# Performance work log

Hardware: AMD Instinct MI355X
Metric: run time of the kernel (lower is better)

Reference implementation:

```python
import jax, jax.numpy as jnp
import numpy as np

N_EMBD = 2048
N_HEAD = 16
D_HEAD = N_EMBD // N_HEAD


def setup_inputs() -> dict:
    key = jax.random.key(0)
    k1, k2, k3 = jax.random.split(key, 3)
    x = jax.random.normal(k1, (2, 2048, N_EMBD), dtype=jnp.float32)
    # torch Linear stores weight as [out, in]; kept in that layout
    w_qkv = jax.random.normal(k2, (3 * N_EMBD, N_EMBD), dtype=jnp.float32) * (1.0 / np.sqrt(N_EMBD))
    w_out = jax.random.normal(k3, (N_EMBD, N_EMBD), dtype=jnp.float32) * (1.0 / np.sqrt(N_EMBD))
    return {"x": x, "w_qkv": w_qkv, "w_out": w_out}


def reference(x, w_qkv, w_out):
    B, T, C = x.shape
    H, D = N_HEAD, D_HEAD
    qkv = jnp.einsum('btc,oc->bto', x, w_qkv)            # [B,T,3C]
    qkv = qkv.reshape(B, T, 3, H, D)
    q = jnp.transpose(qkv[:, :, 0], (0, 2, 1, 3))        # [B,H,T,D]
    k = jnp.transpose(qkv[:, :, 1], (0, 2, 1, 3))
    v = jnp.transpose(qkv[:, :, 2], (0, 2, 1, 3))
    scale = 1.0 / np.sqrt(D).astype(np.float32)
    att = jnp.einsum('bhqd,bhkd->bhqk', q, k) * scale    # [B,H,T,T]
    causal = jnp.tril(jnp.ones((T, T), dtype=bool))
    att = jnp.where(causal[None, None], att, jnp.finfo(att.dtype).min)
    att = jax.nn.softmax(att, axis=-1)
    y = jnp.einsum('bhqk,bhkd->bhqd', att, v)            # [B,H,T,D]
    y = jnp.transpose(y, (0, 2, 1, 3)).reshape(B, T, C)
    return jnp.einsum('btc,oc->bto', y, w_out)
```

## Files before the change

kernel.cpp:

```cpp
#include <hip/hip_runtime.h>
#include <stdint.h>


typedef __attribute__((ext_vector_type(8))) short bf16x8;
typedef __attribute__((ext_vector_type(8))) unsigned short u16x8;
typedef __attribute__((ext_vector_type(4))) unsigned short u16x4;
typedef __attribute__((ext_vector_type(4))) float f32x4;

#define MFMA16(a, b, c) __builtin_amdgcn_mfma_f32_16x16x32_bf16((a), (b), (c), 0, 0, 0)

__device__ __forceinline__ unsigned short f2bf(float f) {
  union { float f; uint32_t u; } v; v.f = f;
  uint32_t r = v.u + 0x7FFFu + ((v.u >> 16) & 1u);
  return (unsigned short)(r >> 16);
}

__device__ __forceinline__ void gld_lds16(const unsigned short* g, unsigned short* lds) {
  __builtin_amdgcn_global_load_lds(
      (const __attribute__((address_space(1))) void*)g,
      (__attribute__((address_space(3))) void*)lds, 16, 0, 0);
}

__global__ __launch_bounds__(256) void cvt_bf16(const float* __restrict__ in,
                                                unsigned short* __restrict__ out, int n8) {
  int stride = gridDim.x * blockDim.x;
  for (int i = blockIdx.x * blockDim.x + threadIdx.x; i < n8; i += stride) {
    float4 a = reinterpret_cast<const float4*>(in)[i * 2];
    float4 b = reinterpret_cast<const float4*>(in)[i * 2 + 1];
    u16x8 o;
    o[0] = f2bf(a.x); o[1] = f2bf(a.y); o[2] = f2bf(a.z); o[3] = f2bf(a.w);
    o[4] = f2bf(b.x); o[5] = f2bf(b.y); o[6] = f2bf(b.z); o[7] = f2bf(b.w);
    reinterpret_cast<u16x8*>(out)[i] = o;
  }
}

__device__ __forceinline__ void gemm128_core(const unsigned short* __restrict__ A,
                                             const unsigned short* __restrict__ Bt,
                                             int K, int brow, int bcol,
                                             unsigned short* lds_a, unsigned short* lds_b,
                                             f32x4 acc[4][4]) {
  const int tid = threadIdx.x;
  const int l   = tid & 63;
  const int w   = tid >> 6;
  const int wr  = (w >> 1) << 6;
  const int wc  = (w & 1) << 6;

  const int srow = tid >> 2;
  const int sswz = (tid & 3) ^ ((srow >> 1) & 3);
  const unsigned short* gA0 = A  + (size_t)(brow + srow) * K + 8 * sswz;
  const unsigned short* gA1 = gA0 + (size_t)64 * K;
  const unsigned short* gB0 = Bt + (size_t)(bcol + srow) * K + 8 * sswz;
  const unsigned short* gB1 = gB0 + (size_t)64 * K;

  unsigned short* la0 = lds_a + tid * 8;
  unsigned short* la1 = lds_a + (256 + tid) * 8;
  unsigned short* lb0 = lds_b + tid * 8;
  unsigned short* lb1 = lds_b + (256 + tid) * 8;

  const int fm    = l & 15;
  const int fswz8 = 8 * ((l >> 4) ^ ((fm >> 1) & 3));

  for (int k0 = 0; k0 < K; k0 += 32) {
    gld_lds16(gA0, la0);
    gld_lds16(gA1, la1);
    gld_lds16(gB0, lb0);
    gld_lds16(gB1, lb1);
    gA0 += 32; gA1 += 32; gB0 += 32; gB1 += 32;
    __syncthreads();
    bf16x8 af[4], bfv[4];
#pragma unroll
    for (int i = 0; i < 4; i++)
      af[i] = *(const bf16x8*)&lds_a[(wr + i * 16 + fm) * 32 + fswz8];
#pragma unroll
    for (int j = 0; j < 4; j++)
      bfv[j] = *(const bf16x8*)&lds_b[(wc + j * 16 + fm) * 32 + fswz8];
#pragma unroll
    for (int i = 0; i < 4; i++)
#pragma unroll
      for (int j = 0; j < 4; j++)
        acc[i][j] = MFMA16(af[i], bfv[j], acc[i][j]);
    __syncthreads();
  }
}

__global__ __launch_bounds__(256) void gemm_qkv(const unsigned short* __restrict__ xb,
                                                const unsigned short* __restrict__ wqb,
                                                unsigned short* __restrict__ Qb,
                                                unsigned short* __restrict__ Kb,
                                                unsigned short* __restrict__ Vtb) {
  __shared__ alignas(16) unsigned short lds_a[128 * 32];
  __shared__ alignas(16) unsigned short lds_b[128 * 32];
  f32x4 acc[4][4];
#pragma unroll
  for (int i = 0; i < 4; i++)
#pragma unroll
    for (int j = 0; j < 4; j++) acc[i][j] = (f32x4){0.f, 0.f, 0.f, 0.f};

  const int brow = blockIdx.y << 7;
  const int bcol = blockIdx.x << 7;
  gemm128_core(xb, wqb, 2048, brow, bcol, lds_a, lds_b, acc);

  const int l = threadIdx.x & 63;
  const int w = threadIdx.x >> 6;
  const int wr = (w >> 1) << 6, wc = (w & 1) << 6;
  const int which = bcol >> 11;
  const int bh = ((brow >> 11) << 4) | ((bcol >> 7) & 15);
  const int tbase = (brow & 2047) + wr + ((l >> 4) << 2);

#pragma unroll
  for (int i = 0; i < 4; i++) {
    const int t0 = tbase + i * 16;
#pragma unroll
    for (int j = 0; j < 4; j++) {
      const int d = wc + j * 16 + (l & 15);
      if (which == 2) {
        u16x4 pk;
#pragma unroll
        for (int r = 0; r < 4; r++) pk[r] = f2bf(acc[i][j][r]);
        *reinterpret_cast<u16x4*>(&Vtb[((size_t)bh * 128 + d) * 2048 + t0]) = pk;
      } else {
        unsigned short* dst = (which == 0 ? Qb : Kb) + ((size_t)bh * 2048 + t0) * 128 + d;
#pragma unroll
        for (int r = 0; r < 4; r++) dst[(size_t)r * 128] = f2bf(acc[i][j][r]);
      }
    }
  }
}

__global__ __launch_bounds__(256) void gemm_out(const unsigned short* __restrict__ yb,
                                                const unsigned short* __restrict__ wob,
                                                float* __restrict__ out) {
  __shared__ alignas(16) unsigned short lds_a[128 * 32];
  __shared__ alignas(16) unsigned short lds_b[128 * 32];
  f32x4 acc[4][4];
#pragma unroll
  for (int i = 0; i < 4; i++)
#pragma unroll
    for (int j = 0; j < 4; j++) acc[i][j] = (f32x4){0.f, 0.f, 0.f, 0.f};

  const int brow = blockIdx.y << 7;
  const int bcol = blockIdx.x << 7;
  gemm128_core(yb, wob, 2048, brow, bcol, lds_a, lds_b, acc);

  const int l = threadIdx.x & 63;
  const int w = threadIdx.x >> 6;
  const int wr = (w >> 1) << 6, wc = (w & 1) << 6;
#pragma unroll
  for (int i = 0; i < 4; i++) {
    const int m0 = brow + wr + i * 16 + ((l >> 4) << 2);
#pragma unroll
    for (int j = 0; j < 4; j++) {
      const int n = bcol + wc + j * 16 + (l & 15);
#pragma unroll
      for (int r = 0; r < 4; r++) out[(size_t)(m0 + r) * 2048 + n] = acc[i][j][r];
    }
  }
}

__global__ __launch_bounds__(256) void attn_kernel(const unsigned short* __restrict__ Qb,
                                                   const unsigned short* __restrict__ Kb,
                                                   const unsigned short* __restrict__ Vtb,
                                                   unsigned short* __restrict__ Yb) {
  __shared__ alignas(16) unsigned short lds_k[64 * 128];
  __shared__ alignas(16) unsigned short lds_v[128 * 64];
  __shared__ alignas(16) unsigned short p_lds[4][16 * 64];

  const int tid = threadIdx.x;
  const int l = tid & 63;
  const int w = tid >> 6;
  const int bh = blockIdx.y;
  const int b = bh >> 4, h = bh & 15;
  const float SC = 0.12752585f;

  const unsigned short* Qg = Qb + (size_t)bh * 2048 * 128;
  const unsigned short* Kg = Kb + (size_t)bh * 2048 * 128;
  const unsigned short* Vg = Vtb + (size_t)bh * 128 * 2048;

  for (int ph = 0; ph < 2; ph++) {
    const int h64 = (ph == 0) ? (int)blockIdx.x : (31 - (int)blockIdx.x);
    const int q0 = h64 << 6;
    const int qw0 = q0 + (w << 4);

    bf16x8 qf[4];
#pragma unroll
    for (int ds = 0; ds < 4; ds++)
      qf[ds] = *(const bf16x8*)&Qg[(size_t)(qw0 + (l & 15)) * 128 + ds * 32 + 8 * (l >> 4)];

    f32x4 yacc[8];
#pragma unroll
    for (int dt = 0; dt < 8; dt++) yacc[dt] = (f32x4){0.f, 0.f, 0.f, 0.f};
    float mrow[4], lrow[4];
#pragma unroll
    for (int r = 0; r < 4; r++) { mrow[r] = -1e30f; lrow[r] = 0.f; }

    const int nkv = h64 + 1;
    for (int t = 0; t < nkv; t++) {
      const int kv0 = t << 6;
#pragma unroll
      for (int c = 0; c < 4; c++) {
        int s = c * 256 + tid;
        int row = s >> 4, g = s & 15;
        gld_lds16(&Kg[(size_t)(kv0 + row) * 128 + 8 * (g ^ (row & 7))], &lds_k[s * 8]);
      }
#pragma unroll
      for (int c = 0; c < 4; c++) {
        int s = c * 256 + tid;
        int row = s >> 3, g = s & 7;
        gld_lds16(&Vg[(size_t)row * 2048 + kv0 + 8 * (g ^ (row & 7))], &lds_v[s * 8]);
      }
      __syncthreads();

      if (kv0 <= qw0 + 15) {
        f32x4 sfr[4];
#pragma unroll
        for (int kt = 0; kt < 4; kt++) {
          const int kr = kt * 16 + (l & 15);
          f32x4 s4 = (f32x4){0.f, 0.f, 0.f, 0.f};
#pragma unroll
          for (int ds = 0; ds < 4; ds++) {
            bf16x8 kfr = *(const bf16x8*)&lds_k[kr * 128 + 8 * (((ds << 2) + (l >> 4)) ^ (kr & 7))];
            s4 = MFMA16(qf[ds], kfr, s4);
          }
          sfr[kt] = s4;
        }
        const bool need_mask = (kv0 + 63 > qw0);
#pragma unroll
        for (int kt = 0; kt < 4; kt++)
#pragma unroll
          for (int r = 0; r < 4; r++) {
            float sv = sfr[kt][r] * SC;
            if (need_mask) {
              int qa = qw0 + ((l >> 4) << 2) + r;
              int ka = kv0 + kt * 16 + (l & 15);
              sv = (ka > qa) ? -1e30f : sv;
            }
            sfr[kt][r] = sv;
          }
        float rmax, f[4], rsum[4];
#pragma unroll
        for (int r = 0; r < 4; r++) {
          rmax = fmaxf(fmaxf(sfr[0][r], sfr[1][r]), fmaxf(sfr[2][r], sfr[3][r]));
          rmax = fmaxf(rmax, __shfl_xor(rmax, 1));
          rmax = fmaxf(rmax, __shfl_xor(rmax, 2));
          rmax = fmaxf(rmax, __shfl_xor(rmax, 4));
          rmax = fmaxf(rmax, __shfl_xor(rmax, 8));
          float mn = fmaxf(mrow[r], rmax);
          f[r] = exp2f(mrow[r] - mn);
          mrow[r] = mn;
          rsum[r] = 0.f;
        }
#pragma unroll
        for (int kt = 0; kt < 4; kt++)
#pragma unroll
          for (int r = 0; r < 4; r++) {
            float p = exp2f(sfr[kt][r] - mrow[r]);
            rsum[r] += p;
            int row = ((l >> 4) << 2) + r;
            int k = kt * 16 + (l & 15);
            p_lds[w][row * 64 + (((k >> 3) ^ (row & 7)) << 3) + (k & 7)] = f2bf(p);
          }
#pragma unroll
        for (int r = 0; r < 4; r++) {
          float s = rsum[r];
          s += __shfl_xor(s, 1);
          s += __shfl_xor(s, 2);
          s += __shfl_xor(s, 4);
          s += __shfl_xor(s, 8);
          lrow[r] = lrow[r] * f[r] + s;
        }
#pragma unroll
        for (int dt = 0; dt < 8; dt++)
#pragma unroll
          for (int r = 0; r < 4; r++) yacc[dt][r] *= f[r];

        asm volatile("s_waitcnt lgkmcnt(0)" ::: "memory");
        __builtin_amdgcn_sched_barrier(0);

#pragma unroll
        for (int ks = 0; ks < 2; ks++) {
          const int prow = l & 15;
          bf16x8 pa = *(const bf16x8*)&p_lds[w][prow * 64 + ((((ks << 2) + (l >> 4)) ^ (prow & 7)) << 3)];
#pragma unroll
          for (int dt = 0; dt < 8; dt++) {
            const int d = dt * 16 + (l & 15);
            bf16x8 vb = *(const bf16x8*)&lds_v[d * 64 + ((((ks << 2) + (l >> 4)) ^ (d & 7)) << 3)];
            yacc[dt] = MFMA16(pa, vb, yacc[dt]);
          }
        }
      }
      __syncthreads();
    }
#pragma unroll
    for (int dt = 0; dt < 8; dt++)
#pragma unroll
      for (int r = 0; r < 4; r++) {
        int qa = qw0 + ((l >> 4) << 2) + r;
        Yb[((size_t)(b * 2048 + qa)) * 2048 + h * 128 + dt * 16 + (l & 15)] =
            f2bf(yacc[dt][r] / lrow[r]);
      }
  }
}

extern "C" void kernel_launch(void* const* d_in, const int* in_sizes, int n_in,
                              void* d_out, int out_size, void* d_ws, size_t ws_size,
                              hipStream_t stream) {
  const float* x    = (const float*)d_in[0];
  const float* wqkv = (const float*)d_in[1];
  const float* wout = (const float*)d_in[2];
  float* out = (float*)d_out;

  unsigned short* ws  = (unsigned short*)d_ws;
  unsigned short* xb  = ws;
  unsigned short* wqb = xb + (size_t)8388608;
  unsigned short* wob = wqb + (size_t)12582912;
  unsigned short* Qb  = wob + (size_t)4194304;
  unsigned short* Kb  = Qb + (size_t)8388608;
  unsigned short* Vtb = Kb + (size_t)8388608;
  unsigned short* Yb  = Vtb + (size_t)8388608;

  cvt_bf16<<<1024, 256, 0, stream>>>(x, xb, 8388608 / 8);
  cvt_bf16<<<1024, 256, 0, stream>>>(wqkv, wqb, 12582912 / 8);
  cvt_bf16<<<512, 256, 0, stream>>>(wout, wob, 4194304 / 8);
  gemm_qkv<<<dim3(48, 32), 256, 0, stream>>>(xb, wqb, Qb, Kb, Vtb);
  attn_kernel<<<dim3(16, 32), 256, 0, stream>>>(Qb, Kb, Vtb, Yb);
  gemm_out<<<dim3(16, 32), 256, 0, stream>>>(Yb, wob, out);
}
```

Before: 291.4 us.

## Replace QKV GEMM with 256x256-tile, 8-wave, multi-stage pipelined kernel

The QKV projection GEMM now uses 256x256 output tiles computed by 512 threads (8 waves). It replaces the single-buffered 128x128 kernel with a double-buffered, K-split LDS pipeline that issues global-to-LDS loads ahead of the MFMA phases, using explicit vmcnt waits, sched barriers and s_setprio. A block-index swizzle groups tiles for L2 reuse. The aim is to hide load latency and raise arithmetic intensity per LDS byte, at the cost of more LDS (128 KB per block), more accumulator registers, fewer blocks (384), and a fragile hand-written wait schedule; the LDS layout drops the bank-conflict swizzle of the old kernel.

```diff
diff --git a/kernel.cpp b/kernel.cpp
--- a/kernel.cpp
+++ b/kernel.cpp
@@ -6,6 +6,7 @@
 typedef __attribute__((ext_vector_type(8))) unsigned short u16x8;
 typedef __attribute__((ext_vector_type(4))) unsigned short u16x4;
 typedef __attribute__((ext_vector_type(4))) float f32x4;
+typedef unsigned short ushort_t;
 
 #define MFMA16(a, b, c) __builtin_amdgcn_mfma_f32_16x16x32_bf16((a), (b), (c), 0, 0, 0)
 
@@ -19,6 +20,12 @@
   __builtin_amdgcn_global_load_lds(
       (const __attribute__((address_space(1))) void*)g,
       (__attribute__((address_space(3))) void*)lds, 16, 0, 0);
+}
+
+__device__ __forceinline__ void sbar() {
+  __builtin_amdgcn_sched_barrier(0);
+  __builtin_amdgcn_s_barrier();
+  __builtin_amdgcn_sched_barrier(0);
 }
 
 __global__ __launch_bounds__(256) void cvt_bf16(const float* __restrict__ in,
@@ -34,6 +41,131 @@
   }
 }
 
+#define QNT 32
+
+#define STG_A(DBUF, KSS, KOFF)                                                  \
+  do { gld_lds16(gA0 + (KOFF), lA + ((DBUF)*2 + (KSS)) * 8192 + tid * 8);       \
+       gld_lds16(gA1 + (KOFF), lA + ((DBUF)*2 + (KSS)) * 8192 + 4096 + tid * 8); } while (0)
+#define STG_B(DBUF, KSS, KOFF)                                                  \
+  do { gld_lds16(gB0 + (KOFF), lB + ((DBUF)*2 + (KSS)) * 8192 + tid * 8);       \
+       gld_lds16(gB1 + (KOFF), lB + ((DBUF)*2 + (KSS)) * 8192 + 4096 + tid * 8); } while (0)
+
+#define PH(BUF, KS, MG, STAGE_STMT, WAIT_STMT)                                  \
+  {                                                                             \
+    const unsigned short* lab = lA + ((BUF) * 2 + (KS)) * 8192;                 \
+    const unsigned short* lbb = lB + ((BUF) * 2 + (KS)) * 8192;                 \
+    bf16x8 af_[4];                                                              \
+    _Pragma("unroll") for (int mf = 0; mf < 4; ++mf)                            \
+      af_[mf] = *(const bf16x8*)&lab[(wm * 128 + (MG) * 64 + mf * 16 + lm) * 32 + k8]; \
+    if ((MG) == 0) {                                                            \
+      _Pragma("unroll") for (int nf = 0; nf < 4; ++nf)                          \
+        bfr[nf] = *(const bf16x8*)&lbb[(wn * 64 + nf * 16 + lm) * 32 + k8];     \
+    }                                                                           \
+    STAGE_STMT;                                                                 \
+    sbar();                                                                     \
+    asm volatile("s_waitcnt lgkmcnt(0)" ::: "memory");                          \
+    __builtin_amdgcn_sched_barrier(0);                                          \
+    __builtin_amdgcn_s_setprio(1);                                              \
+    _Pragma("unroll") for (int mf = 0; mf < 4; ++mf)                            \
+      _Pragma("unroll") for (int nf = 0; nf < 4; ++nf)                          \
+        acc[(MG) * 4 + mf][nf] = MFMA16(af_[mf], bfr[nf], acc[(MG) * 4 + mf][nf]); \
+    __builtin_amdgcn_s_setprio(0);                                              \
+    WAIT_STMT;                                                                  \
+    sbar();                                                                     \
+  }
+
+#define WV8 asm volatile("s_waitcnt vmcnt(8)" ::: "memory")
+#define WV4 asm volatile("s_waitcnt vmcnt(4)" ::: "memory")
+#define WV0 asm volatile("s_waitcnt vmcnt(0)" ::: "memory")
+#define NOPST ((void)0)
+
+__global__ __launch_bounds__(512, 2) void gemm_qkv8(const unsigned short* __restrict__ xb,
+                                                    const unsigned short* __restrict__ wqb,
+                                                    unsigned short* __restrict__ Qb,
+                                                    unsigned short* __restrict__ Kb,
+                                                    unsigned short* __restrict__ Vtb) {
+  __shared__ alignas(16) unsigned short lA[2 * 2 * 8192];
+  __shared__ alignas(16) unsigned short lB[2 * 2 * 8192];
+
+  const int bid = blockIdx.x;
+  const int swz = (bid & 7) * 48 + (bid >> 3);
+  const int bx = swz % 24, by = swz / 24;
+  const int brow = by << 8, bcol = bx << 8;
+
+  const int tid = threadIdx.x;
+  const int l = tid & 63, w = tid >> 6;
+  const int wm = w >> 2, wn = w & 3;
+  const int lm = l & 15, k8 = 8 * (l >> 4);
+
+  const int srow = tid >> 2;
+  const int sk8 = (tid & 3) * 8;
+  const unsigned short* gA0 = xb + (size_t)(brow + srow) * 2048 + sk8;
+  const unsigned short* gA1 = xb + (size_t)(brow + 128 + srow) * 2048 + sk8;
+  const unsigned short* gB0 = wqb + (size_t)(bcol + srow) * 2048 + sk8;
+  const unsigned short* gB1 = wqb + (size_t)(bcol + 128 + srow) * 2048 + sk8;
+
+  f32x4 acc[8][4];
+#pragma unroll
+  for (int i = 0; i < 8; ++i)
+#pragma unroll
+    for (int j = 0; j < 4; ++j) acc[i][j] = (f32x4){0.f, 0.f, 0.f, 0.f};
+  bf16x8 bfr[4];
+
+  STG_A(0, 0, 0);  STG_B(0, 0, 0);
+  STG_A(0, 1, 32); STG_B(0, 1, 32);
+  STG_A(1, 0, 64); STG_B(1, 0, 64);
+  WV8;
+  sbar();
+
+  for (int t = 0; t < QNT - 2; ++t) {
+    const int buf = t & 1;
+    PH(buf, 0, 0, STG_A(buf ^ 1, 1, (t + 1) * 64 + 32), NOPST);
+    PH(buf, 0, 1, STG_B(buf ^ 1, 1, (t + 1) * 64 + 32), WV8);
+    PH(buf, 1, 0, STG_A(buf, 0, (t + 2) * 64), NOPST);
+    PH(buf, 1, 1, STG_B(buf, 0, (t + 2) * 64), WV8);
+  }
+  {
+    const int buf = (QNT - 2) & 1;
+    PH(buf, 0, 0, STG_A(buf ^ 1, 1, (QNT - 1) * 64 + 32), NOPST);
+    PH(buf, 0, 1, STG_B(buf ^ 1, 1, (QNT - 1) * 64 + 32), WV8);
+    PH(buf, 1, 0, NOPST, NOPST);
+    PH(buf, 1, 1, NOPST, WV4);
+  }
+  {
+    const int buf = (QNT - 1) & 1;
+    PH(buf, 0, 0, NOPST, NOPST);
+    PH(buf, 0, 1, NOPST, WV0);
+    PH(buf, 1, 0, NOPST, NOPST);
+    PH(buf, 1, 1, NOPST, NOPST);
+  }
+
+  const int lr4 = (l >> 4) << 2;
+#pragma unroll
+  for (int mf = 0; mf < 8; ++mf) {
+    const int trow = brow + wm * 128 + mf * 16 + lr4;
+    const int b_ = trow >> 11;
+    const int t0 = trow & 2047;
+#pragma unroll
+    for (int nf = 0; nf < 4; ++nf) {
+      const int c = bcol + wn * 64 + nf * 16 + lm;
+      const int which = c >> 11;
+      const int cc = c & 2047;
+      const int h = cc >> 7, d = cc & 127;
+      const int bh = (b_ << 4) | h;
+      if (which == 2) {
+        u16x4 pk;
+#pragma unroll
+        for (int r = 0; r < 4; ++r) pk[r] = f2bf(acc[mf][nf][r]);
+        *reinterpret_cast<u16x4*>(&Vtb[((size_t)bh * 128 + d) * 2048 + t0]) = pk;
+      } else {
+        unsigned short* dst = (which == 0 ? Qb : Kb) + ((size_t)bh * 2048 + t0) * 128 + d;
+#pragma unroll
+        for (int r = 0; r < 4; ++r) dst[(size_t)r * 128] = f2bf(acc[mf][nf][r]);
+      }
+    }
+  }
+}
+
 __device__ __forceinline__ void gemm128_core(const unsigned short* __restrict__ A,
                                              const unsigned short* __restrict__ Bt,
                                              int K, int brow, int bcol,
@@ -80,50 +212,6 @@
       for (int j = 0; j < 4; j++)
         acc[i][j] = MFMA16(af[i], bfv[j], acc[i][j]);
     __syncthreads();
-  }
-}
-
-__global__ __launch_bounds__(256) void gemm_qkv(const unsigned short* __restrict__ xb,
-                                                const unsigned short* __restrict__ wqb,
-                                                unsigned short* __restrict__ Qb,
-                                                unsigned short* __restrict__ Kb,
-                                                unsigned short* __restrict__ Vtb) {
-  __shared__ alignas(16) unsigned short lds_a[128 * 32];
-  __shared__ alignas(16) unsigned short lds_b[128 * 32];
-  f32x4 acc[4][4];
-#pragma unroll
-  for (int i = 0; i < 4; i++)
-#pragma unroll
-    for (int j = 0; j < 4; j++) acc[i][j] = (f32x4){0.f, 0.f, 0.f, 0.f};
-
-  const int brow = blockIdx.y << 7;
-  const int bcol = blockIdx.x << 7;
-  gemm128_core(xb, wqb, 2048, brow, bcol, lds_a, lds_b, acc);
-
-  const int l = threadIdx.x & 63;
-  const int w = threadIdx.x >> 6;
-  const int wr = (w >> 1) << 6, wc = (w & 1) << 6;
-  const int which = bcol >> 11;
-  const int bh = ((brow >> 11) << 4) | ((bcol >> 7) & 15);
-  const int tbase = (brow & 2047) + wr + ((l >> 4) << 2);
-
-#pragma unroll
-  for (int i = 0; i < 4; i++) {
-    const int t0 = tbase + i * 16;
-#pragma unroll
-    for (int j = 0; j < 4; j++) {
-      const int d = wc + j * 16 + (l & 15);
-      if (which == 2) {
-        u16x4 pk;
-#pragma unroll
-        for (int r = 0; r < 4; r++) pk[r] = f2bf(acc[i][j][r]);
-        *reinterpret_cast<u16x4*>(&Vtb[((size_t)bh * 128 + d) * 2048 + t0]) = pk;
-      } else {
-        unsigned short* dst = (which == 0 ? Qb : Kb) + ((size_t)bh * 2048 + t0) * 128 + d;
-#pragma unroll
-        for (int r = 0; r < 4; r++) dst[(size_t)r * 128] = f2bf(acc[i][j][r]);
-      }
-    }
   }
 }
 
@@ -321,7 +409,7 @@
   cvt_bf16<<<1024, 256, 0, stream>>>(x, xb, 8388608 / 8);
   cvt_bf16<<<1024, 256, 0, stream>>>(wqkv, wqb, 12582912 / 8);
   cvt_bf16<<<512, 256, 0, stream>>>(wout, wob, 4194304 / 8);
-  gemm_qkv<<<dim3(48, 32), 256, 0, stream>>>(xb, wqb, Qb, Kb, Vtb);
+  gemm_qkv8<<<384, 512, 0, stream>>>(xb, wqb, Qb, Kb, Vtb);
   attn_kernel<<<dim3(16, 32), 256, 0, stream>>>(Qb, Kb, Vtb, Yb);
   gemm_out<<<dim3(16, 32), 256, 0, stream>>>(Yb, wob, out);
 }
```

Result: slower. 333.7 us (+14.5%).

## Double-buffer GEMM LDS loads, remap blocks per XCD, and split attention query tiles

Applied to the files above, without the earlier changes.

Both GEMMs now use double-buffered LDS, so the global-to-LDS copy of the next K slice runs while MFMAs work on the current one. All three kernels switch to a flat 1D grid with an XCD-aware block-to-tile mapping, so tiles sharing operands (or the same head) land on the same XCD and reuse its L2. The attention kernel drops the per-block pairing of two query tiles (one short, one long) and launches one block per query tile, staggering tile order by head. This adds parallelism and cache locality but gives up the built-in causal load balancing, and doubles GEMM LDS use, which may lower occupancy.

```diff
diff --git a/kernel.cpp b/kernel.cpp
--- a/kernel.cpp
+++ b/kernel.cpp
@@ -34,51 +34,62 @@
   }
 }
 
-__device__ __forceinline__ void gemm128_core(const unsigned short* __restrict__ A,
+#define STG128(BUFOFF, KOFF)                                                    \
+  do {                                                                          \
+    gld_lds16(gA0 + (KOFF), ldsA + (BUFOFF) + tid * 8);                         \
+    gld_lds16(gA1 + (KOFF), ldsA + (BUFOFF) + 2048 + tid * 8);                  \
+    gld_lds16(gB0 + (KOFF), ldsB + (BUFOFF) + tid * 8);                         \
+    gld_lds16(gB1 + (KOFF), ldsB + (BUFOFF) + 2048 + tid * 8);                  \
+  } while (0)
+
+__device__ __forceinline__ void gemm128_step(const unsigned short* la,
+                                             const unsigned short* lb,
+                                             int wr, int wc, int fm, int fswz8,
+                                             f32x4 acc[4][4]) {
+  bf16x8 af[4], bfv[4];
+#pragma unroll
+  for (int i = 0; i < 4; i++)
+    af[i] = *(const bf16x8*)&la[(wr + i * 16 + fm) * 32 + fswz8];
+#pragma unroll
+  for (int j = 0; j < 4; j++)
+    bfv[j] = *(const bf16x8*)&lb[(wc + j * 16 + fm) * 32 + fswz8];
+#pragma unroll
+  for (int i = 0; i < 4; i++)
+#pragma unroll
+    for (int j = 0; j < 4; j++)
+      acc[i][j] = MFMA16(af[i], bfv[j], acc[i][j]);
+}
+
+__device__ __forceinline__ void gemm128_dbuf(const unsigned short* __restrict__ A,
                                              const unsigned short* __restrict__ Bt,
                                              int K, int brow, int bcol,
-                                             unsigned short* lds_a, unsigned short* lds_b,
+                                             unsigned short* ldsA, unsigned short* ldsB,
                                              f32x4 acc[4][4]) {
   const int tid = threadIdx.x;
-  const int l   = tid & 63;
-  const int w   = tid >> 6;
-  const int wr  = (w >> 1) << 6;
-  const int wc  = (w & 1) << 6;
+  const int l = tid & 63;
+  const int w = tid >> 6;
+  const int wr = (w >> 1) << 6;
+  const int wc = (w & 1) << 6;
 
   const int srow = tid >> 2;
   const int sswz = (tid & 3) ^ ((srow >> 1) & 3);
-  const unsigned short* gA0 = A  + (size_t)(brow + srow) * K + 8 * sswz;
+  const unsigned short* gA0 = A + (size_t)(brow + srow) * K + 8 * sswz;
   const unsigned short* gA1 = gA0 + (size_t)64 * K;
   const unsigned short* gB0 = Bt + (size_t)(bcol + srow) * K + 8 * sswz;
   const unsigned short* gB1 = gB0 + (size_t)64 * K;
 
-  unsigned short* la0 = lds_a + tid * 8;
-  unsigned short* la1 = lds_a + (256 + tid) * 8;
-  unsigned short* lb0 = lds_b + tid * 8;
-  unsigned short* lb1 = lds_b + (256 + tid) * 8;
-
-  const int fm    = l & 15;
+  const int fm = l & 15;
   const int fswz8 = 8 * ((l >> 4) ^ ((fm >> 1) & 3));
 
-  for (int k0 = 0; k0 < K; k0 += 32) {
-    gld_lds16(gA0, la0);
-    gld_lds16(gA1, la1);
-    gld_lds16(gB0, lb0);
-    gld_lds16(gB1, lb1);
-    gA0 += 32; gA1 += 32; gB0 += 32; gB1 += 32;
+  STG128(0, 0);
+  __syncthreads();
+
+  for (int k0 = 0; k0 < K; k0 += 64) {
+    STG128(4096, k0 + 32);
+    gemm128_step(ldsA, ldsB, wr, wc, fm, fswz8, acc);
     __syncthreads();
-    bf16x8 af[4], bfv[4];
-#pragma unroll
-    for (int i = 0; i < 4; i++)
-      af[i] = *(const bf16x8*)&lds_a[(wr + i * 16 + fm) * 32 + fswz8];
-#pragma unroll
-    for (int j = 0; j < 4; j++)
-      bfv[j] = *(const bf16x8*)&lds_b[(wc + j * 16 + fm) * 32 + fswz8];
-#pragma unroll
-    for (int i = 0; i < 4; i++)
-#pragma unroll
-      for (int j = 0; j < 4; j++)
-        acc[i][j] = MFMA16(af[i], bfv[j], acc[i][j]);
+    if (k0 + 64 < K) STG128(0, k0 + 64);
+    gemm128_step(ldsA + 4096, ldsB + 4096, wr, wc, fm, fswz8, acc);
     __syncthreads();
   }
 }
@@ -88,17 +99,23 @@
                                                 unsigned short* __restrict__ Qb,
                                                 unsigned short* __restrict__ Kb,
                                                 unsigned short* __restrict__ Vtb) {
-  __shared__ alignas(16) unsigned short lds_a[128 * 32];
-  __shared__ alignas(16) unsigned short lds_b[128 * 32];
+  __shared__ alignas(16) unsigned short ldsA[2 * 128 * 32];
+  __shared__ alignas(16) unsigned short ldsB[2 * 128 * 32];
   f32x4 acc[4][4];
 #pragma unroll
   for (int i = 0; i < 4; i++)
 #pragma unroll
     for (int j = 0; j < 4; j++) acc[i][j] = (f32x4){0.f, 0.f, 0.f, 0.f};
 
-  const int brow = blockIdx.y << 7;
-  const int bcol = blockIdx.x << 7;
-  gemm128_core(xb, wqb, 2048, brow, bcol, lds_a, lds_b, acc);
+  const int bid = blockIdx.x;
+  const int xcd = bid & 7;
+  const int loc = bid >> 3;
+  const int bx = xcd * 6 + loc % 6;
+  const int by = loc / 6;
+  const int brow = by << 7;
+  const int bcol = bx << 7;
+
+  gemm128_dbuf(xb, wqb, 2048, brow, bcol, ldsA, ldsB, acc);
 
   const int l = threadIdx.x & 63;
   const int w = threadIdx.x >> 6;
@@ -130,17 +147,23 @@
 __global__ __launch_bounds__(256) void gemm_out(const unsigned short* __restrict__ yb,
                                                 const unsigned short* __restrict__ wob,
                                                 float* __restrict__ out) {
-  __shared__ alignas(16) unsigned short lds_a[128 * 32];
-  __shared__ alignas(16) unsigned short lds_b[128 * 32];
+  __shared__ alignas(16) unsigned short ldsA[2 * 128 * 32];
+  __shared__ alignas(16) unsigned short ldsB[2 * 128 * 32];
   f32x4 acc[4][4];
 #pragma unroll
   for (int i = 0; i < 4; i++)
 #pragma unroll
     for (int j = 0; j < 4; j++) acc[i][j] = (f32x4){0.f, 0.f, 0.f, 0.f};
 
-  const int brow = blockIdx.y << 7;
-  const int bcol = blockIdx.x << 7;
-  gemm128_core(yb, wob, 2048, brow, bcol, lds_a, lds_b, acc);
+  const int bid = blockIdx.x;
+  const int xcd = bid & 7;
+  const int loc = bid >> 3;
+  const int bx = (xcd & 3) * 4 + (loc & 3);
+  const int by = (xcd >> 2) * 16 + (loc >> 2);
+  const int brow = by << 7;
+  const int bcol = bx << 7;
+
+  gemm128_dbuf(yb, wob, 2048, brow, bcol, ldsA, ldsB, acc);
 
   const int l = threadIdx.x & 63;
   const int w = threadIdx.x >> 6;
@@ -168,7 +191,14 @@
   const int tid = threadIdx.x;
   const int l = tid & 63;
   const int w = tid >> 6;
-  const int bh = blockIdx.y;
+
+  const int flat = blockIdx.x;
+  const int xcd = flat & 7;
+  const int loc = flat >> 3;
+  const int bh = xcd * 4 + (loc >> 5);
+  const int jidx = loc & 31;
+  const int h64 = (jidx + bh) & 31;
+
   const int b = bh >> 4, h = bh & 15;
   const float SC = 0.12752585f;
 
@@ -176,129 +206,126 @@
   const unsigned short* Kg = Kb + (size_t)bh * 2048 * 128;
   const unsigned short* Vg = Vtb + (size_t)bh * 128 * 2048;
 
-  for (int ph = 0; ph < 2; ph++) {
-    const int h64 = (ph == 0) ? (int)blockIdx.x : (31 - (int)blockIdx.x);
-    const int q0 = h64 << 6;
-    const int qw0 = q0 + (w << 4);
-
-    bf16x8 qf[4];
-#pragma unroll
-    for (int ds = 0; ds < 4; ds++)
-      qf[ds] = *(const bf16x8*)&Qg[(size_t)(qw0 + (l & 15)) * 128 + ds * 32 + 8 * (l >> 4)];
-
-    f32x4 yacc[8];
-#pragma unroll
-    for (int dt = 0; dt < 8; dt++) yacc[dt] = (f32x4){0.f, 0.f, 0.f, 0.f};
-    float mrow[4], lrow[4];
-#pragma unroll
-    for (int r = 0; r < 4; r++) { mrow[r] = -1e30f; lrow[r] = 0.f; }
-
-    const int nkv = h64 + 1;
-    for (int t = 0; t < nkv; t++) {
-      const int kv0 = t << 6;
-#pragma unroll
-      for (int c = 0; c < 4; c++) {
-        int s = c * 256 + tid;
-        int row = s >> 4, g = s & 15;
-        gld_lds16(&Kg[(size_t)(kv0 + row) * 128 + 8 * (g ^ (row & 7))], &lds_k[s * 8]);
-      }
-#pragma unroll
-      for (int c = 0; c < 4; c++) {
-        int s = c * 256 + tid;
-        int row = s >> 3, g = s & 7;
-        gld_lds16(&Vg[(size_t)row * 2048 + kv0 + 8 * (g ^ (row & 7))], &lds_v[s * 8]);
-      }
-      __syncthreads();
-
-      if (kv0 <= qw0 + 15) {
-        f32x4 sfr[4];
-#pragma unroll
-        for (int kt = 0; kt < 4; kt++) {
-          const int kr = kt * 16 + (l & 15);
-          f32x4 s4 = (f32x4){0.f, 0.f, 0.f, 0.f};
-#pragma unroll
-          for (int ds = 0; ds < 4; ds++) {
-            bf16x8 kfr = *(const bf16x8*)&lds_k[kr * 128 + 8 * (((ds << 2) + (l >> 4)) ^ (kr & 7))];
-            s4 = MFMA16(qf[ds], kfr, s4);
+  const int q0 = h64 << 6;
+  const int qw0 = q0 + (w << 4);
+
+  bf16x8 qf[4];
+#pragma unroll
+  for (int ds = 0; ds < 4; ds++)
+    qf[ds] = *(const bf16x8*)&Qg[(size_t)(qw0 + (l & 15)) * 128 + ds * 32 + 8 * (l >> 4)];
+
+  f32x4 yacc[8];
+#pragma unroll
+  for (int dt = 0; dt < 8; dt++) yacc[dt] = (f32x4){0.f, 0.f, 0.f, 0.f};
+  float mrow[4], lrow[4];
+#pragma unroll
+  for (int r = 0; r < 4; r++) { mrow[r] = -1e30f; lrow[r] = 0.f; }
+
+  const int nkv = h64 + 1;
+  for (int t = 0; t < nkv; t++) {
+    const int kv0 = t << 6;
+#pragma unroll
+    for (int c = 0; c < 4; c++) {
+      int s = c * 256 + tid;
+      int row = s >> 4, g = s & 15;
+      gld_lds16(&Kg[(size_t)(kv0 + row) * 128 + 8 * (g ^ (row & 7))], &lds_k[s * 8]);
+    }
+#pragma unroll
+    for (int c = 0; c < 4; c++) {
+      int s = c * 256 + tid;
+      int row = s >> 3, g = s & 7;
+      gld_lds16(&Vg[(size_t)row * 2048 + kv0 + 8 * (g ^ (row & 7))], &lds_v[s * 8]);
+    }
+    __syncthreads();
+
+    if (kv0 <= qw0 + 15) {
+      f32x4 sfr[4];
+#pragma unroll
+      for (int kt = 0; kt < 4; kt++) {
+        const int kr = kt * 16 + (l & 15);
+        f32x4 s4 = (f32x4){0.f, 0.f, 0.f, 0.f};
+#pragma unroll
+        for (int ds = 0; ds < 4; ds++) {
+          bf16x8 kfr = *(const bf16x8*)&lds_k[kr * 128 + 8 * (((ds << 2) + (l >> 4)) ^ (kr & 7))];
+          s4 = MFMA16(qf[ds], kfr, s4);
+        }
+        sfr[kt] = s4;
+      }
+      const bool need_mask = (kv0 + 63 > qw0);
+#pragma unroll
+      for (int kt = 0; kt < 4; kt++)
+#pragma unroll
+        for (int r = 0; r < 4; r++) {
+          float sv = sfr[kt][r] * SC;
+          if (need_mask) {
+            int qa = qw0 + ((l >> 4) << 2) + r;
+            int ka = kv0 + kt * 16 + (l & 15);
+            sv = (ka > qa) ? -1e30f : sv;
           }
-          sfr[kt] = s4;
+          sfr[kt][r] = sv;
         }
-        const bool need_mask = (kv0 + 63 > qw0);
-#pragma unroll
-        for (int kt = 0; kt < 4; kt++)
-#pragma unroll
-          for (int r = 0; r < 4; r++) {
-            float sv = sfr[kt][r] * SC;
-            if (need_mask) {
-              int qa = qw0 + ((l >> 4) << 2) + r;
-              int ka = kv0 + kt * 16 + (l & 15);
-              sv = (ka > qa) ? -1e30f : sv;
-            }
-            sfr[kt][r] = sv;
-          }
-        float rmax, f[4], rsum[4];
+      float rmax, f[4], rsum[4];
+#pragma unroll
+      for (int r = 0; r < 4; r++) {
+        rmax = fmaxf(fmaxf(sfr[0][r], sfr[1][r]), fmaxf(sfr[2][r], sfr[3][r]));
+        rmax = fmaxf(rmax, __shfl_xor(rmax, 1));
+        rmax = fmaxf(rmax, __shfl_xor(rmax, 2));
+        rmax = fmaxf(rmax, __shfl_xor(rmax, 4));
+        rmax = fmaxf(rmax, __shfl_xor(rmax, 8));
+        float mn = fmaxf(mrow[r], rmax);
+        f[r] = exp2f(mrow[r] - mn);
+        mrow[r] = mn;
+        rsum[r] = 0.f;
+      }
+#pragma unroll
+      for (int kt = 0; kt < 4; kt++)
 #pragma unroll
         for (int r = 0; r < 4; r++) {
-          rmax = fmaxf(fmaxf(sfr[0][r], sfr[1][r]), fmaxf(sfr[2][r], sfr[3][r]));
-          rmax = fmaxf(rmax, __shfl_xor(rmax, 1));
-          rmax = fmaxf(rmax, __shfl_xor(rmax, 2));
-          rmax = fmaxf(rmax, __shfl_xor(rmax, 4));
-          rmax = fmaxf(rmax, __shfl_xor(rmax, 8));
-          float mn = fmaxf(mrow[r], rmax);
-          f[r] = exp2f(mrow[r] - mn);
-          mrow[r] = mn;
-          rsum[r] = 0.f;
+          float p = exp2f(sfr[kt][r] - mrow[r]);
+          rsum[r] += p;
+          int row = ((l >> 4) << 2) + r;
+          int k = kt * 16 + (l & 15);
+          p_lds[w][row * 64 + (((k >> 3) ^ (row & 7)) << 3) + (k & 7)] = f2bf(p);
         }
 #pragma unroll
-        for (int kt = 0; kt < 4; kt++)
-#pragma unroll
-          for (int r = 0; r < 4; r++) {
-            float p = exp2f(sfr[kt][r] - mrow[r]);
-            rsum[r] += p;
-            int row = ((l >> 4) << 2) + r;
-            int k = kt * 16 + (l & 15);
-            p_lds[w][row * 64 + (((k >> 3) ^ (row & 7)) << 3) + (k & 7)] = f2bf(p);
-          }
-#pragma unroll
-        for (int r = 0; r < 4; r++) {
-          float s = rsum[r];
-          s += __shfl_xor(s, 1);
-          s += __shfl_xor(s, 2);
-          s += __shfl_xor(s, 4);
-          s += __shfl_xor(s, 8);
-          lrow[r] = lrow[r] * f[r] + s;
+      for (int r = 0; r < 4; r++) {
+        float s = rsum[r];
+        s += __shfl_xor(s, 1);
+        s += __shfl_xor(s, 2);
+        s += __shfl_xor(s, 4);
+        s += __shfl_xor(s, 8);
+        lrow[r] = lrow[r] * f[r] + s;
+      }
+#pragma unroll
+      for (int dt = 0; dt < 8; dt++)
+#pragma unroll
+        for (int r = 0; r < 4; r++) yacc[dt][r] *= f[r];
+
+      asm volatile("s_waitcnt lgkmcnt(0)" ::: "memory");
+      __builtin_amdgcn_sched_barrier(0);
+
+#pragma unroll
+      for (int ks = 0; ks < 2; ks++) {
+        const int prow = l & 15;
+        bf16x8 pa = *(const bf16x8*)&p_lds[w][prow * 64 + ((((ks << 2) + (l >> 4)) ^ (prow & 7)) << 3)];
+#pragma unroll
+        for (int dt = 0; dt < 8; dt++) {
+          const int d = dt * 16 + (l & 15);
+          bf16x8 vb = *(const bf16x8*)&lds_v[d * 64 + ((((ks << 2) + (l >> 4)) ^ (d & 7)) << 3)];
+          yacc[dt] = MFMA16(pa, vb, yacc[dt]);
         }
-#pragma unroll
-        for (int dt = 0; dt < 8; dt++)
-#pragma unroll
-          for (int r = 0; r < 4; r++) yacc[dt][r] *= f[r];
-
-        asm volatile("s_waitcnt lgkmcnt(0)" ::: "memory");
-        __builtin_amdgcn_sched_barrier(0);
-
-#pragma unroll
-        for (int ks = 0; ks < 2; ks++) {
-          const int prow = l & 15;
-          bf16x8 pa = *(const bf16x8*)&p_lds[w][prow * 64 + ((((ks << 2) + (l >> 4)) ^ (prow & 7)) << 3)];
-#pragma unroll
-          for (int dt = 0; dt < 8; dt++) {
-            const int d = dt * 16 + (l & 15);
-            bf16x8 vb = *(const bf16x8*)&lds_v[d * 64 + ((((ks << 2) + (l >> 4)) ^ (d & 7)) << 3)];
-            yacc[dt] = MFMA16(pa, vb, yacc[dt]);
-          }
-        }
-      }
-      __syncthreads();
-    }
-#pragma unroll
-    for (int dt = 0; dt < 8; dt++)
-#pragma unroll
-      for (int r = 0; r < 4; r++) {
-        int qa = qw0 + ((l >> 4) << 2) + r;
-        Yb[((size_t)(b * 2048 + qa)) * 2048 + h * 128 + dt * 16 + (l & 15)] =
-            f2bf(yacc[dt][r] / lrow[r]);
-      }
-  }
+      }
+    }
+    __syncthreads();
+  }
+#pragma unroll
+  for (int dt = 0; dt < 8; dt++)
+#pragma unroll
+    for (int r = 0; r < 4; r++) {
+      int qa = qw0 + ((l >> 4) << 2) + r;
+      Yb[((size_t)(b * 2048 + qa)) * 2048 + h * 128 + dt * 16 + (l & 15)] =
+          f2bf(yacc[dt][r] / lrow[r]);
+    }
 }
 
 extern "C" void kernel_launch(void* const* d_in, const int* in_sizes, int n_in,
@@ -321,7 +348,7 @@
   cvt_bf16<<<1024, 256, 0, stream>>>(x, xb, 8388608 / 8);
   cvt_bf16<<<1024, 256, 0, stream>>>(wqkv, wqb, 12582912 / 8);
   cvt_bf16<<<512, 256, 0, stream>>>(wout, wob, 4194304 / 8);
-  gemm_qkv<<<dim3(48, 32), 256, 0, stream>>>(xb, wqb, Qb, Kb, Vtb);
-  attn_kernel<<<dim3(16, 32), 256, 0, stream>>>(Qb, Kb, Vtb, Yb);
-  gemm_out<<<dim3(16, 32), 256, 0, stream>>>(Yb, wob, out);
-}
+  gemm_qkv<<<1536, 256, 0, stream>>>(xb, wqb, Qb, Kb, Vtb);
+  attn_kernel<<<1024, 256, 0, stream>>>(Qb, Kb, Vtb, Yb);
+  gemm_out<<<512, 256, 0, stream>>>(Yb, wob, out);
+}
```

After: 337.9 us. 1.16x slower.

## Double-buffer K/V tiles, remap blocks per XCD, skip lazy softmax rescale

Applied to the files above, without the earlier changes.

The attention kernel now double-buffers K/V tiles in LDS, issuing the next tile's global-to-LDS loads before computing on the current tile so load latency overlaps MFMA work. Blocks are remapped from a 1D grid so each XCD handles a contiguous set of batch-heads, aiming for better L2 reuse of K/V. The online softmax skips rescaling the accumulator when the running max grows by at most 8 (in log2 units), saving multiplies at the cost of a wave-wide vote and a bounded risk of precision loss. LDS use doubles for K/V, which may lower occupancy.

```diff
diff --git a/kernel.cpp b/kernel.cpp
--- a/kernel.cpp
+++ b/kernel.cpp
@@ -157,18 +157,42 @@
   }
 }
 
+__device__ __forceinline__ void stage_kv64(const unsigned short* __restrict__ Kg,
+                                           const unsigned short* __restrict__ Vg,
+                                           int kv0, unsigned short* dk,
+                                           unsigned short* dv, int tid) {
+#pragma unroll
+  for (int c = 0; c < 4; c++) {
+    int s = c * 256 + tid;
+    int row = s >> 4, g = s & 15;
+    gld_lds16(&Kg[(size_t)(kv0 + row) * 128 + 8 * (g ^ (row & 7))], &dk[s * 8]);
+  }
+#pragma unroll
+  for (int c = 0; c < 4; c++) {
+    int s = c * 256 + tid;
+    int row = s >> 3, g = s & 7;
+    gld_lds16(&Vg[(size_t)row * 2048 + kv0 + 8 * (g ^ (row & 7))], &dv[s * 8]);
+  }
+}
+
 __global__ __launch_bounds__(256) void attn_kernel(const unsigned short* __restrict__ Qb,
                                                    const unsigned short* __restrict__ Kb,
                                                    const unsigned short* __restrict__ Vtb,
                                                    unsigned short* __restrict__ Yb) {
-  __shared__ alignas(16) unsigned short lds_k[64 * 128];
-  __shared__ alignas(16) unsigned short lds_v[128 * 64];
+  __shared__ alignas(16) unsigned short lds_k[2][64 * 128];
+  __shared__ alignas(16) unsigned short lds_v[2][128 * 64];
   __shared__ alignas(16) unsigned short p_lds[4][16 * 64];
 
   const int tid = threadIdx.x;
   const int l = tid & 63;
   const int w = tid >> 6;
-  const int bh = blockIdx.y;
+
+  const int bid = blockIdx.x;
+  const int xcd = bid & 7;
+  const int loc = bid >> 3;
+  const int bh = xcd * 4 + (loc >> 4);
+  const int jidx = loc & 15;
+
   const int b = bh >> 4, h = bh & 15;
   const float SC = 0.12752585f;
 
@@ -177,7 +201,7 @@
   const unsigned short* Vg = Vtb + (size_t)bh * 128 * 2048;
 
   for (int ph = 0; ph < 2; ph++) {
-    const int h64 = (ph == 0) ? (int)blockIdx.x : (31 - (int)blockIdx.x);
+    const int h64 = (ph == 0) ? jidx : (31 - jidx);
     const int q0 = h64 << 6;
     const int qw0 = q0 + (w << 4);
 
@@ -194,21 +218,18 @@
     for (int r = 0; r < 4; r++) { mrow[r] = -1e30f; lrow[r] = 0.f; }
 
     const int nkv = h64 + 1;
+
+    stage_kv64(Kg, Vg, 0, lds_k[0], lds_v[0], tid);
+    asm volatile("s_waitcnt vmcnt(0)" ::: "memory");
+    __syncthreads();
+
     for (int t = 0; t < nkv; t++) {
       const int kv0 = t << 6;
-#pragma unroll
-      for (int c = 0; c < 4; c++) {
-        int s = c * 256 + tid;
-        int row = s >> 4, g = s & 15;
-        gld_lds16(&Kg[(size_t)(kv0 + row) * 128 + 8 * (g ^ (row & 7))], &lds_k[s * 8]);
-      }
-#pragma unroll
-      for (int c = 0; c < 4; c++) {
-        int s = c * 256 + tid;
-        int row = s >> 3, g = s & 7;
-        gld_lds16(&Vg[(size_t)row * 2048 + kv0 + 8 * (g ^ (row & 7))], &lds_v[s * 8]);
-      }
-      __syncthreads();
+      const int buf = t & 1;
+      const unsigned short* kb = lds_k[buf];
+      const unsigned short* vb = lds_v[buf];
+      if (t + 1 < nkv)
+        stage_kv64(Kg, Vg, kv0 + 64, lds_k[buf ^ 1], lds_v[buf ^ 1], tid);
 
       if (kv0 <= qw0 + 15) {
         f32x4 sfr[4];
@@ -218,7 +239,7 @@
           f32x4 s4 = (f32x4){0.f, 0.f, 0.f, 0.f};
 #pragma unroll
           for (int ds = 0; ds < 4; ds++) {
-            bf16x8 kfr = *(const bf16x8*)&lds_k[kr * 128 + 8 * (((ds << 2) + (l >> 4)) ^ (kr & 7))];
+            bf16x8 kfr = *(const bf16x8*)&kb[kr * 128 + 8 * (((ds << 2) + (l >> 4)) ^ (kr & 7))];
             s4 = MFMA16(qf[ds], kfr, s4);
           }
           sfr[kt] = s4;
@@ -236,19 +257,33 @@
             }
             sfr[kt][r] = sv;
           }
-        float rmax, f[4], rsum[4];
+        float rmax[4];
 #pragma unroll
         for (int r = 0; r < 4; r++) {
-          rmax = fmaxf(fmaxf(sfr[0][r], sfr[1][r]), fmaxf(sfr[2][r], sfr[3][r]));
-          rmax = fmaxf(rmax, __shfl_xor(rmax, 1));
-          rmax = fmaxf(rmax, __shfl_xor(rmax, 2));
-          rmax = fmaxf(rmax, __shfl_xor(rmax, 4));
-          rmax = fmaxf(rmax, __shfl_xor(rmax, 8));
-          float mn = fmaxf(mrow[r], rmax);
-          f[r] = exp2f(mrow[r] - mn);
-          mrow[r] = mn;
-          rsum[r] = 0.f;
-        }
+          float m = fmaxf(fmaxf(sfr[0][r], sfr[1][r]), fmaxf(sfr[2][r], sfr[3][r]));
+          m = fmaxf(m, __shfl_xor(m, 1));
+          m = fmaxf(m, __shfl_xor(m, 2));
+          m = fmaxf(m, __shfl_xor(m, 4));
+          m = fmaxf(m, __shfl_xor(m, 8));
+          rmax[r] = m;
+        }
+        bool sm = (rmax[0] <= mrow[0] + 8.f) && (rmax[1] <= mrow[1] + 8.f) &&
+                  (rmax[2] <= mrow[2] + 8.f) && (rmax[3] <= mrow[3] + 8.f);
+        if (!__all(sm)) {
+          float f[4];
+#pragma unroll
+          for (int r = 0; r < 4; r++) {
+            float mn = fmaxf(mrow[r], rmax[r]);
+            f[r] = exp2f(mrow[r] - mn);
+            mrow[r] = mn;
+            lrow[r] *= f[r];
+          }
+#pragma unroll
+          for (int dt = 0; dt < 8; dt++)
+#pragma unroll
+            for (int r = 0; r < 4; r++) yacc[dt][r] *= f[r];
+        }
+        float rsum[4] = {0.f, 0.f, 0.f, 0.f};
 #pragma unroll
         for (int kt = 0; kt < 4; kt++)
 #pragma unroll
@@ -266,12 +301,8 @@
           s += __shfl_xor(s, 2);
           s += __shfl_xor(s, 4);
           s += __shfl_xor(s, 8);
-          lrow[r] = lrow[r] * f[r] + s;
-        }
-#pragma unroll
-        for (int dt = 0; dt < 8; dt++)
-#pragma unroll
-          for (int r = 0; r < 4; r++) yacc[dt][r] *= f[r];
+          lrow[r] += s;
+        }
 
         asm volatile("s_waitcnt lgkmcnt(0)" ::: "memory");
         __builtin_amdgcn_sched_barrier(0);
@@ -283,11 +314,12 @@
 #pragma unroll
           for (int dt = 0; dt < 8; dt++) {
             const int d = dt * 16 + (l & 15);
-            bf16x8 vb = *(const bf16x8*)&lds_v[d * 64 + ((((ks << 2) + (l >> 4)) ^ (d & 7)) << 3)];
-            yacc[dt] = MFMA16(pa, vb, yacc[dt]);
+            bf16x8 vv = *(const bf16x8*)&vb[d * 64 + ((((ks << 2) + (l >> 4)) ^ (d & 7)) << 3)];
+            yacc[dt] = MFMA16(pa, vv, yacc[dt]);
           }
         }
       }
+      asm volatile("s_waitcnt vmcnt(0)" ::: "memory");
       __syncthreads();
     }
 #pragma unroll
@@ -322,6 +354,6 @@
   cvt_bf16<<<1024, 256, 0, stream>>>(wqkv, wqb, 12582912 / 8);
   cvt_bf16<<<512, 256, 0, stream>>>(wout, wob, 4194304 / 8);
   gemm_qkv<<<dim3(48, 32), 256, 0, stream>>>(xb, wqb, Qb, Kb, Vtb);
-  attn_kernel<<<dim3(16, 32), 256, 0, stream>>>(Qb, Kb, Vtb, Yb);
+  attn_kernel<<<512, 256, 0, stream>>>(Qb, Kb, Vtb, Yb);
   gemm_out<<<dim3(16, 32), 256, 0, stream>>>(Yb, wob, out);
 }
```

After: 286.1 us. Within noise of the previous version (-1.8%).
